# Optimization experiments

Hardware: AMD Instinct MI355X
Metric: run time of the kernel (lower is better)

Reference implementation:

```python
import jax, jax.numpy as jnp
import numpy as np
import math

B, S, D, H = 4, 2048, 1024, 16
HD = D // H  # head_dim = 64


def setup_inputs() -> dict:
    key = jax.random.key(0)
    ks = jax.random.split(key, 7)
    s = 0.02
    return {
        "q": jax.random.normal(ks[0], (B, S, D), jnp.float32),
        "k": jax.random.normal(ks[1], (B, S, D), jnp.float32),
        "v": jax.random.normal(ks[2], (B, S, D), jnp.float32),
        "wq": jax.random.normal(ks[3], (D, D), jnp.float32) * s,
        "wk": jax.random.normal(ks[4], (D, D), jnp.float32) * s,
        "wv": jax.random.normal(ks[5], (D, D), jnp.float32) * s,
        "wo": jax.random.normal(ks[6], (D, D), jnp.float32) * s,
    }


def reference(q, k, v, wq, wk, wv, wo):
    # Linear (no bias): y = x @ W.T, W is (out, in)
    xq = jnp.einsum('bsd,ed->bse', q, wq).reshape(B, S, H, HD).transpose(0, 2, 1, 3)
    xk = jnp.einsum('bsd,ed->bse', k, wk).reshape(B, S, H, HD).transpose(0, 2, 1, 3)
    xv = jnp.einsum('bsd,ed->bse', v, wv).reshape(B, S, H, HD).transpose(0, 2, 1, 3)
    scores = jnp.einsum('bhqd,bhkd->bhqk', xq, xk) / math.sqrt(HD)  # [B,H,S,S]
    causal = jnp.tril(jnp.ones((S, S), dtype=bool))
    scores = jnp.where(causal[None, None], scores, jnp.float32(-jnp.inf))
    probs = jax.nn.softmax(scores, axis=-1)  # dropout p=0 -> identity
    out = jnp.einsum('bhqk,bhkd->bhqd', probs, xv)  # [B,H,S,HD]
    out = out.transpose(0, 2, 1, 3).reshape(B, S, D)
    return jnp.einsum('bsd,ed->bse', out, wo)
```

## Files before the change

kernel.cpp:

```cpp
#include <hip/hip_runtime.h>

#define SS 2048
#define DD 1024
#define HH 16
#define HD 64
#define MM 8192

typedef unsigned short ushort_t;
typedef __attribute__((ext_vector_type(8))) short short8;
typedef __attribute__((ext_vector_type(4))) float f32x4;
typedef __attribute__((ext_vector_type(4))) unsigned short us4;
typedef __attribute__((ext_vector_type(8))) unsigned short us8;

__device__ __forceinline__ ushort_t f2bf(float f) {
    union { float f; unsigned u; } x; x.f = f;
    unsigned r = x.u + 0x7fffu + ((x.u >> 16) & 1u);
    return (ushort_t)(r >> 16);
}
__device__ __forceinline__ float bf2f(ushort_t h) {
    union { unsigned u; float f; } x; x.u = ((unsigned)h) << 16; return x.f;
}
__device__ __forceinline__ unsigned pack_bf2(float a, float b) {
    union { float f; unsigned u; } x, y; x.f = a; y.f = b;
    return __builtin_amdgcn_perm(y.u, x.u, 0x07060302u);
}

__device__ __forceinline__ void async16(const void* g, void* l) {
    __builtin_amdgcn_global_load_lds(
        (const __attribute__((address_space(1))) unsigned int*)g,
        (__attribute__((address_space(3))) unsigned int*)l, 16, 0, 0);
}

__global__ void cvt_all(const float* __restrict__ q, const float* __restrict__ k,
                        const float* __restrict__ v, const float* __restrict__ wq,
                        const float* __restrict__ wk, const float* __restrict__ wv,
                        const float* __restrict__ wo, ushort_t* __restrict__ qbf,
                        ushort_t* __restrict__ kbf, ushort_t* __restrict__ vbf,
                        ushort_t* __restrict__ wbf) {
    long i = ((long)blockIdx.x * 256 + threadIdx.x) * 8;
    const float* src; ushort_t* dst;
    if (i < (3l << 23)) {
        int s = (int)(i >> 23);
        long off = i & ((1l << 23) - 1);
        src = ((s == 0) ? q : (s == 1) ? k : v) + off;
        dst = ((s == 0) ? qbf : (s == 1) ? kbf : vbf) + off;
    } else {
        long j = i - (3l << 23);
        int s = (int)(j >> 20);
        src = ((s == 0) ? wq : (s == 1) ? wk : (s == 2) ? wv : wo) + (j & 1048575);
        dst = wbf + j;
    }
    float4 f0 = *(const float4*)src;
    float4 f1 = *(const float4*)(src + 4);
    us8 o;
    o[0] = f2bf(f0.x); o[1] = f2bf(f0.y); o[2] = f2bf(f0.z); o[3] = f2bf(f0.w);
    o[4] = f2bf(f1.x); o[5] = f2bf(f1.y); o[6] = f2bf(f1.z); o[7] = f2bf(f1.w);
    *(us8*)dst = o;
}

__device__ __forceinline__ void epi_scatter(f32x4 acc[4][4], int m0, int n0,
                                            int mode, void* Yv) {
    int tid = threadIdx.x;
    int w = tid >> 6, lane = tid & 63;
    int l16 = lane & 15, quad = lane >> 4;
    int wm = (w >> 1) * 64, wn = (w & 1) * 64;
    #pragma unroll
    for (int mt = 0; mt < 4; ++mt) {
        #pragma unroll
        for (int r = 0; r < 4; ++r) {
            int row = m0 + wm + mt * 16 + quad * 4 + r;
            #pragma unroll
            for (int nt = 0; nt < 4; ++nt) {
                int col = n0 + wn + nt * 16 + l16;
                float vf = acc[mt][nt][r];
                if (mode == 2) {
                    ((float*)Yv)[(size_t)row * DD + col] = vf;
                } else {
                    ushort_t vh = f2bf(vf);
                    int b = row >> 11, s = row & 2047;
                    int h = col >> 6,  hd = col & 63;
                    if (mode == 0) {
                        ((ushort_t*)Yv)[(((size_t)b * HH + h) * SS + s) * HD + hd] = vh;
                    } else {
                        int sp = (s & ~63) | (((s & 15) << 2) | ((s >> 4) & 3));
                        ((ushort_t*)Yv)[(((size_t)b * HH + h) * HD + hd) * SS + sp] = vh;
                    }
                }
            }
        }
    }
}

__global__ __launch_bounds__(256) void proj3f(const ushort_t* __restrict__ qbf,
                                              const ushort_t* __restrict__ kbf,
                                              const ushort_t* __restrict__ vbf,
                                              const ushort_t* __restrict__ Wall,
                                              ushort_t* __restrict__ xq,
                                              ushort_t* __restrict__ xk,
                                              ushort_t* __restrict__ xvT) {
    __shared__ __align__(16) ushort_t As[2][128 * 32];
    __shared__ __align__(16) ushort_t Bs[2][128 * 32];
    int tid = threadIdx.x;
    int w = tid >> 6, lane = tid & 63;
    int l16 = lane & 15, quad = lane >> 4;
    int mat   = (int)(blockIdx.x >> 9);
    int inner = (int)(blockIdx.x & 511);
    int m0 = (inner & 63) * 128;
    int n0 = (inner >> 6) * 128;
    const ushort_t* A  = (mat == 0) ? qbf : (mat == 1) ? kbf : vbf;
    const ushort_t* Bw = Wall + ((size_t)mat << 20);
    int wm = (w >> 1) * 64, wn = (w & 1) * 64;

    f32x4 acc[4][4];
    #pragma unroll
    for (int i = 0; i < 4; ++i)
        #pragma unroll
        for (int j = 0; j < 4; ++j) acc[i][j] = (f32x4){0.f, 0.f, 0.f, 0.f};

    int g0 = w * 64 + lane, r0 = g0 >> 2, j0 = ((g0 & 3) ^ (r0 & 3)) * 8;
    int g1 = g0 + 256,      r1 = g1 >> 2, j1 = ((g1 & 3) ^ (r1 & 3)) * 8;
    int swA = (quad ^ (l16 & 3)) * 8;

    async16(A  + (size_t)(m0 + r0) * DD + j0, &As[0][(size_t)(w * 64) * 8]);
    async16(A  + (size_t)(m0 + r1) * DD + j1, &As[0][(size_t)(256 + w * 64) * 8]);
    async16(Bw + (size_t)(n0 + r0) * DD + j0, &Bs[0][(size_t)(w * 64) * 8]);
    async16(Bw + (size_t)(n0 + r1) * DD + j1, &Bs[0][(size_t)(256 + w * 64) * 8]);

    for (int kk = 0; kk < 32; ++kk) {
        int c = kk & 1;
        __syncthreads();
        if (kk < 31) {
            int k1 = (kk + 1) * 32;
            async16(A  + (size_t)(m0 + r0) * DD + k1 + j0, &As[c ^ 1][(size_t)(w * 64) * 8]);
            async16(A  + (size_t)(m0 + r1) * DD + k1 + j1, &As[c ^ 1][(size_t)(256 + w * 64) * 8]);
            async16(Bw + (size_t)(n0 + r0) * DD + k1 + j0, &Bs[c ^ 1][(size_t)(w * 64) * 8]);
            async16(Bw + (size_t)(n0 + r1) * DD + k1 + j1, &Bs[c ^ 1][(size_t)(256 + w * 64) * 8]);
        }
        short8 af[4], bfr[4];
        #pragma unroll
        for (int t = 0; t < 4; ++t) {
            af[t]  = *(const short8*)&As[c][(wm + t * 16 + l16) * 32 + swA];
            bfr[t] = *(const short8*)&Bs[c][(wn + t * 16 + l16) * 32 + swA];
        }
        #pragma unroll
        for (int mt = 0; mt < 4; ++mt)
            #pragma unroll
            for (int nt = 0; nt < 4; ++nt)
                acc[mt][nt] = __builtin_amdgcn_mfma_f32_16x16x32_bf16(af[mt], bfr[nt], acc[mt][nt], 0, 0, 0);
    }

    void* Y = (mat == 0) ? (void*)xq : (mat == 1) ? (void*)xk : (void*)xvT;
    epi_scatter(acc, m0, n0, (mat == 2) ? 1 : 0, Y);
}

__global__ __launch_bounds__(512) void out_gemm(const ushort_t* __restrict__ Abf,
                                                const ushort_t* __restrict__ Bw,
                                                float* __restrict__ Y) {
    __shared__ __align__(16) ushort_t As[2][256 * 32];
    __shared__ __align__(16) ushort_t Bs[2][128 * 32];
    int tid = threadIdx.x;
    int w = tid >> 6, lane = tid & 63;
    int l16 = lane & 15, quad = lane >> 4;
    int inner = (int)blockIdx.x;
    int m0 = (inner & 31) * 256;
    int n0 = (inner >> 5) * 128;
    int wm = (w >> 1) * 64, wn = (w & 1) * 64;

    f32x4 acc[4][4];
    #pragma unroll
    for (int i = 0; i < 4; ++i)
        #pragma unroll
        for (int j = 0; j < 4; ++j) acc[i][j] = (f32x4){0.f, 0.f, 0.f, 0.f};

    int ra0 = tid >> 2,           ja0 = ((tid & 3) ^ (ra0 & 3)) * 8;
    int ga1 = tid + 512;
    int ra1 = ga1 >> 2,           ja1 = ((ga1 & 3) ^ (ra1 & 3)) * 8;
    int rb  = tid >> 2,           jb  = ((tid & 3) ^ (rb & 3)) * 8;
    int swA = (quad ^ (l16 & 3)) * 8;

    async16(Abf + (size_t)(m0 + ra0) * DD + ja0, &As[0][(size_t)(w * 64) * 8]);
    async16(Abf + (size_t)(m0 + ra1) * DD + ja1, &As[0][(size_t)(512 + w * 64) * 8]);
    async16(Bw  + (size_t)(n0 + rb)  * DD + jb,  &Bs[0][(size_t)(w * 64) * 8]);

    for (int kk = 0; kk < 32; ++kk) {
        int c = kk & 1;
        __syncthreads();
        if (kk < 31) {
            int k1 = (kk + 1) * 32;
            async16(Abf + (size_t)(m0 + ra0) * DD + k1 + ja0, &As[c ^ 1][(size_t)(w * 64) * 8]);
            async16(Abf + (size_t)(m0 + ra1) * DD + k1 + ja1, &As[c ^ 1][(size_t)(512 + w * 64) * 8]);
            async16(Bw  + (size_t)(n0 + rb)  * DD + k1 + jb,  &Bs[c ^ 1][(size_t)(w * 64) * 8]);
        }
        short8 af[4], bfr[4];
        #pragma unroll
        for (int t = 0; t < 4; ++t) {
            af[t]  = *(const short8*)&As[c][(wm + t * 16 + l16) * 32 + swA];
            bfr[t] = *(const short8*)&Bs[c][(wn + t * 16 + l16) * 32 + swA];
        }
        #pragma unroll
        for (int mt = 0; mt < 4; ++mt)
            #pragma unroll
            for (int nt = 0; nt < 4; ++nt)
                acc[mt][nt] = __builtin_amdgcn_mfma_f32_16x16x32_bf16(af[mt], bfr[nt], acc[mt][nt], 0, 0, 0);
    }
    epi_scatter(acc, m0, n0, 2, Y);
}

__global__ __launch_bounds__(256) void attn_kernel(const ushort_t* __restrict__ xq,
                                                   const ushort_t* __restrict__ xk,
                                                   const ushort_t* __restrict__ xvT,
                                                   ushort_t* __restrict__ ao) {
    __shared__ __align__(16) ushort_t Ksm[2][64 * 64];
    __shared__ __align__(16) ushort_t Vsm[2][64 * 64];
    __shared__ __align__(16) ushort_t Psm[4][16 * 72];

    int tid = threadIdx.x;
    int w = tid >> 6, lane = tid & 63;
    int l16 = lane & 15, quad = lane >> 4;
    int bh = blockIdx.x & 63;
    int p  = blockIdx.x >> 6;
    int b = bh >> 4, h = bh & 15;

    const ushort_t* Q  = xq  + (size_t)bh * SS * HD;
    const ushort_t* K  = xk  + (size_t)bh * SS * HD;
    const ushort_t* VT = xvT + (size_t)bh * HD * SS;

    int g0 = w * 64 + lane, r0 = g0 >> 3, j0 = ((g0 & 7) ^ (r0 & 7)) * 8;
    int g1 = g0 + 256,      r1 = g1 >> 3, j1 = ((g1 & 7) ^ (r1 & 7)) * 8;

    short8 ones;
    #pragma unroll
    for (int i = 0; i < 8; ++i) ones[i] = (short)0x3F80;

    const float CS = 0.125f * 1.44269504f;

    for (int ph = 0; ph < 2; ++ph) {
        int qt = ph ? (31 - p) : p;
        int qb = qt * 64;
        int qmin = qb + w * 16;

        short8 aq[2];
        #pragma unroll
        for (int kc = 0; kc < 2; ++kc) {
            short8 t = *(const short8*)(Q + (size_t)(qmin + l16) * HD + kc * 32 + quad * 8);
            #pragma unroll
            for (int i = 0; i < 8; ++i)
                t[i] = (short)f2bf(bf2f((ushort_t)t[i]) * CS);
            aq[kc] = t;
        }

        f32x4 o[4];
        #pragma unroll
        for (int dt = 0; dt < 4; ++dt) o[dt] = (f32x4){0.f, 0.f, 0.f, 0.f};
        f32x4 lacc = (f32x4){0.f, 0.f, 0.f, 0.f};

        __syncthreads();
        async16(K  + (size_t)r0 * HD + j0, &Ksm[0][(size_t)(w * 64) * 8]);
        async16(K  + (size_t)r1 * HD + j1, &Ksm[0][(size_t)(256 + w * 64) * 8]);
        async16(VT + (size_t)r0 * SS + j0, &Vsm[0][(size_t)(w * 64) * 8]);
        async16(VT + (size_t)r1 * SS + j1, &Vsm[0][(size_t)(256 + w * 64) * 8]);

        for (int kt = 0; kt <= qt; ++kt) {
            int kb = kt * 64;
            int c = kt & 1;
            __syncthreads();
            if (kt < qt) {
                int kb1 = kb + 64;
                async16(K  + (size_t)(kb1 + r0) * HD + j0, &Ksm[c ^ 1][(size_t)(w * 64) * 8]);
                async16(K  + (size_t)(kb1 + r1) * HD + j1, &Ksm[c ^ 1][(size_t)(256 + w * 64) * 8]);
                async16(VT + (size_t)r0 * SS + kb1 + j0, &Vsm[c ^ 1][(size_t)(w * 64) * 8]);
                async16(VT + (size_t)r1 * SS + kb1 + j1, &Vsm[c ^ 1][(size_t)(256 + w * 64) * 8]);
            }

            f32x4 sc[4];
            __builtin_amdgcn_s_setprio(1);
            #pragma unroll
            for (int nt = 0; nt < 4; ++nt) {
                int row = nt * 16 + l16;
                short8 bk0 = *(const short8*)&Ksm[c][row * 64 + ((0 + quad) ^ (l16 & 7)) * 8];
                short8 bk1 = *(const short8*)&Ksm[c][row * 64 + ((4 + quad) ^ (l16 & 7)) * 8];
                f32x4 cc = (f32x4){0.f, 0.f, 0.f, 0.f};
                cc = __builtin_amdgcn_mfma_f32_16x16x32_bf16(aq[0], bk0, cc, 0, 0, 0);
                cc = __builtin_amdgcn_mfma_f32_16x16x32_bf16(aq[1], bk1, cc, 0, 0, 0);
                sc[nt] = cc;
            }
            __builtin_amdgcn_s_setprio(0);

            bool msk = (kt == qt);
            #pragma unroll
            for (int r = 0; r < 4; ++r) {
                float e0, e1, e2, e3;
                if (msk) {
                    int qg = qmin + quad * 4 + r;
                    e0 = (kb +  0 + l16 <= qg) ? __builtin_amdgcn_exp2f(sc[0][r]) : 0.f;
                    e1 = (kb + 16 + l16 <= qg) ? __builtin_amdgcn_exp2f(sc[1][r]) : 0.f;
                    e2 = (kb + 32 + l16 <= qg) ? __builtin_amdgcn_exp2f(sc[2][r]) : 0.f;
                    e3 = (kb + 48 + l16 <= qg) ? __builtin_amdgcn_exp2f(sc[3][r]) : 0.f;
                } else {
                    e0 = __builtin_amdgcn_exp2f(sc[0][r]);
                    e1 = __builtin_amdgcn_exp2f(sc[1][r]);
                    e2 = __builtin_amdgcn_exp2f(sc[2][r]);
                    e3 = __builtin_amdgcn_exp2f(sc[3][r]);
                }
                uint2 pk = { pack_bf2(e0, e1), pack_bf2(e2, e3) };
                *(uint2*)&Psm[w][(quad * 4 + r) * 72 + l16 * 4] = pk;
            }

            asm volatile("s_waitcnt lgkmcnt(0)" ::: "memory");

            __builtin_amdgcn_s_setprio(1);
            #pragma unroll
            for (int kc = 0; kc < 2; ++kc) {
                short8 ap = *(const short8*)&Psm[w][l16 * 72 + kc * 32 + quad * 8];
                lacc = __builtin_amdgcn_mfma_f32_16x16x32_bf16(ap, ones, lacc, 0, 0, 0);
                #pragma unroll
                for (int dt = 0; dt < 4; ++dt) {
                    int row = dt * 16 + l16;
                    short8 bv = *(const short8*)&Vsm[c][row * 64 + ((kc * 4 + quad) ^ (l16 & 7)) * 8];
                    o[dt] = __builtin_amdgcn_mfma_f32_16x16x32_bf16(ap, bv, o[dt], 0, 0, 0);
                }
            }
            __builtin_amdgcn_s_setprio(0);
        }

        #pragma unroll
        for (int r = 0; r < 4; ++r) {
            float inv = 1.0f / lacc[r];
            int qg = qmin + quad * 4 + r;
            #pragma unroll
            for (int dt = 0; dt < 4; ++dt)
                ao[((size_t)(b * SS + qg)) * DD + h * HD + dt * 16 + l16] = f2bf(o[dt][r] * inv);
        }
    }
}

extern "C" void kernel_launch(void* const* d_in, const int* in_sizes, int n_in,
                              void* d_out, int out_size, void* d_ws, size_t ws_size,
                              hipStream_t stream) {
    const float* q  = (const float*)d_in[0];
    const float* k  = (const float*)d_in[1];
    const float* v  = (const float*)d_in[2];
    const float* wq = (const float*)d_in[3];
    const float* wk = (const float*)d_in[4];
    const float* wv = (const float*)d_in[5];
    const float* wo = (const float*)d_in[6];
    float* out = (float*)d_out;

    ushort_t* wbf = (ushort_t*)d_ws;
    ushort_t* xq  = wbf + 4194304ull;
    ushort_t* xk  = xq  + 8388608ull;
    ushort_t* xvT = xk  + 8388608ull;
    ushort_t* ao  = xvT + 8388608ull;
    ushort_t* vbf = ao;
    ushort_t* qbf = (ushort_t*)d_out;
    ushort_t* kbf = qbf + 8388608ull;

    cvt_all<<<14336, 256, 0, stream>>>(q, k, v, wq, wk, wv, wo, qbf, kbf, vbf, wbf);
    proj3f<<<1536, 256, 0, stream>>>(qbf, kbf, vbf, wbf, xq, xk, xvT);
    attn_kernel<<<1024, 256, 0, stream>>>(xq, xk, xvT, ao);
    out_gemm<<<256, 512, 0, stream>>>(ao, wbf + 3145728ull, out);
}
```

Baseline: 339.3 us.

## Triple-buffer QKV projection GEMM with explicit vmcnt waits and barriers

Converts the projection GEMM's double-buffered async global-to-LDS loads into a three-stage ring that prefetches two K-steps ahead. Each step waits only for the loads of the tile being consumed, using explicit vmcnt counts and raw s_barrier in place of __syncthreads. The goal is to hide more global memory latency behind the MFMA work. In exchange LDS use per block rises by half, which may lower occupancy, and correctness now depends on the hand-counted vmcnt values matching the loads actually in flight.

```diff
diff --git a/kernel.cpp b/kernel.cpp
--- a/kernel.cpp
+++ b/kernel.cpp
@@ -98,8 +98,8 @@
                                               ushort_t* __restrict__ xq,
                                               ushort_t* __restrict__ xk,
                                               ushort_t* __restrict__ xvT) {
-    __shared__ __align__(16) ushort_t As[2][128 * 32];
-    __shared__ __align__(16) ushort_t Bs[2][128 * 32];
+    __shared__ __align__(16) ushort_t As[3][128 * 32];
+    __shared__ __align__(16) ushort_t Bs[3][128 * 32];
     int tid = threadIdx.x;
     int w = tid >> 6, lane = tid & 63;
     int l16 = lane & 15, quad = lane >> 4;
@@ -121,21 +121,39 @@
     int g1 = g0 + 256,      r1 = g1 >> 2, j1 = ((g1 & 3) ^ (r1 & 3)) * 8;
     int swA = (quad ^ (l16 & 3)) * 8;
 
-    async16(A  + (size_t)(m0 + r0) * DD + j0, &As[0][(size_t)(w * 64) * 8]);
-    async16(A  + (size_t)(m0 + r1) * DD + j1, &As[0][(size_t)(256 + w * 64) * 8]);
-    async16(Bw + (size_t)(n0 + r0) * DD + j0, &Bs[0][(size_t)(w * 64) * 8]);
-    async16(Bw + (size_t)(n0 + r1) * DD + j1, &Bs[0][(size_t)(256 + w * 64) * 8]);
-
+    const ushort_t* Ar0 = A  + (size_t)(m0 + r0) * DD + j0;
+    const ushort_t* Ar1 = A  + (size_t)(m0 + r1) * DD + j1;
+    const ushort_t* Br0 = Bw + (size_t)(n0 + r0) * DD + j0;
+    const ushort_t* Br1 = Bw + (size_t)(n0 + r1) * DD + j1;
+    int ldsA0 = w * 64 * 8, ldsA1 = (256 + w * 64) * 8;
+
+    async16(Ar0,      &As[0][ldsA0]);
+    async16(Ar1,      &As[0][ldsA1]);
+    async16(Br0,      &Bs[0][ldsA0]);
+    async16(Br1,      &Bs[0][ldsA1]);
+    async16(Ar0 + 32, &As[1][ldsA0]);
+    async16(Ar1 + 32, &As[1][ldsA1]);
+    async16(Br0 + 32, &Bs[1][ldsA0]);
+    async16(Br1 + 32, &Bs[1][ldsA1]);
+
+    int c = 0, c2 = 2;
     for (int kk = 0; kk < 32; ++kk) {
-        int c = kk & 1;
-        __syncthreads();
-        if (kk < 31) {
-            int k1 = (kk + 1) * 32;
-            async16(A  + (size_t)(m0 + r0) * DD + k1 + j0, &As[c ^ 1][(size_t)(w * 64) * 8]);
-            async16(A  + (size_t)(m0 + r1) * DD + k1 + j1, &As[c ^ 1][(size_t)(256 + w * 64) * 8]);
-            async16(Bw + (size_t)(n0 + r0) * DD + k1 + j0, &Bs[c ^ 1][(size_t)(w * 64) * 8]);
-            async16(Bw + (size_t)(n0 + r1) * DD + k1 + j1, &Bs[c ^ 1][(size_t)(256 + w * 64) * 8]);
-        }
+        __builtin_amdgcn_s_barrier();
+        if (kk < 30) {
+            int k2 = (kk + 2) * 32;
+            async16(Ar0 + k2, &As[c2][ldsA0]);
+            async16(Ar1 + k2, &As[c2][ldsA1]);
+            async16(Br0 + k2, &Bs[c2][ldsA0]);
+            async16(Br1 + k2, &Bs[c2][ldsA1]);
+            asm volatile("s_waitcnt vmcnt(8)" ::: "memory");
+        } else if (kk == 30) {
+            asm volatile("s_waitcnt vmcnt(4)" ::: "memory");
+        } else {
+            asm volatile("s_waitcnt vmcnt(0)" ::: "memory");
+        }
+        __builtin_amdgcn_s_barrier();
+        __builtin_amdgcn_sched_barrier(0);
+
         short8 af[4], bfr[4];
         #pragma unroll
         for (int t = 0; t < 4; ++t) {
@@ -147,6 +165,9 @@
             #pragma unroll
             for (int nt = 0; nt < 4; ++nt)
                 acc[mt][nt] = __builtin_amdgcn_mfma_f32_16x16x32_bf16(af[mt], bfr[nt], acc[mt][nt], 0, 0, 0);
+
+        c  = (c  == 2) ? 0 : c  + 1;
+        c2 = (c2 == 2) ? 0 : c2 + 1;
     }
 
     void* Y = (mat == 0) ? (void*)xq : (mat == 1) ? (void*)xk : (void*)xvT;
```

Result: no change. 343.5 us (+1.2%).
